# Performance work log

Hardware: AMD Instinct MI355X
Metric: run time of the kernel (lower is better)

The kernel has to match this reference:

```python
import jax, jax.numpy as jnp
import numpy as np

B, R, D, P = 32, 512, 256, 5532  # images, rois/image, feat dim, num_pids
NEG_INF = -1e30

def setup_inputs() -> dict:
    key = jax.random.key(0)
    k1, k2, k3 = jax.random.split(key, 3)
    inputs = jax.random.normal(k1, (B * R, D), dtype=jnp.float32)
    cls_scores = jax.random.uniform(k2, (B * R, 1), dtype=jnp.float32)
    roi_label = jax.random.randint(k3, (B, R), 0, P + 1)  # 0 = background -> label -1
    return {"inputs": inputs, "cls_scores": cls_scores, "roi_label": roi_label}

def reference(inputs, cls_scores, roi_label):
    x = (inputs * cls_scores).reshape(B, R, D)          # scale features by cls score
    label = roi_label - 1                               # [B,R], -1 = background
    valid = label >= 0                                  # keep labeled ROIs only
    lbl = jnp.where(valid, label, 0)

    # per-image per-pid mean prototypes via one segmented reduction
    seg = (jnp.arange(B)[:, None] * P + lbl).reshape(-1)             # [B*R]
    w = valid.reshape(-1).astype(x.dtype)
    sums = jax.ops.segment_sum(x.reshape(-1, D) * w[:, None], seg, num_segments=B * P)
    counts = jax.ops.segment_sum(w, seg, num_segments=B * P)          # [B*P]
    proto = sums / jnp.maximum(counts, 1.0)[:, None]
    proto = proto / jnp.maximum(jnp.linalg.norm(proto, axis=-1, keepdims=True), 1e-12)
    proto = jax.lax.stop_gradient(proto).reshape(B, P, D)            # .detach() in torch
    present = (counts > 0).reshape(B, P)                              # unique labels per image

    # project each ROI feature onto its image's prototypes
    logits = jnp.einsum('brd,bpd->brp', x, proto)                     # [B,R,P]
    logits = jnp.where(present[:, None, :], logits, NEG_INF)          # softmax over unique labels only
    logp = jax.nn.log_softmax(logits, axis=-1)
    nll = -jnp.take_along_axis(logp, lbl[..., None], axis=-1)[..., 0] # [B,R]
    nll = jnp.where(valid, nll, 0.0)
    n_valid = jnp.maximum(jnp.sum(valid).astype(x.dtype), 1.0)
    return jnp.sum(nll) / n_valid
```

## Files before the change

### kernel.cpp

```cpp
#include <hip/hip_runtime.h>
#include <math.h>

#define Bn 32
#define Rn 512
#define Dn 256
#define Pn 5532
#define MAXU 512

typedef short short8 __attribute__((ext_vector_type(8)));
typedef short short4v __attribute__((ext_vector_type(4)));
typedef float floatx4 __attribute__((ext_vector_type(4)));

#define XBF_OFF    0
#define XBF_WORDS  (Bn*Rn*Dn/2)
#define PBF_OFF    (XBF_OFF + XBF_WORDS)
#define PBF_WORDS  (Bn*MAXU*Dn/2)
#define LBLC_OFF   (PBF_OFF + PBF_WORDS)
#define NUNIQ_OFF  (LBLC_OFF + Bn*Rn)
#define NVALID_OFF (NUNIQ_OFF + 32)
#define SEXP_OFF   (NVALID_OFF + 32)
#define NLL_OFF    (SEXP_OFF + Bn*Rn)
#define TK2_OFF    (NLL_OFF + 1)
#define TICK_OFF   (TK2_OFF + 1)
#define ZEROW      (Bn*Rn + 2 + 128)

__device__ __forceinline__ unsigned short bf16r(float f) {
    union { float f; unsigned int u; } c; c.f = f;
    return (unsigned short)((c.u + 0x7FFFu + ((c.u >> 16) & 1u)) >> 16);
}

__device__ __forceinline__ void async16(void* lds, const void* g) {
    auto* l3 = reinterpret_cast<__attribute__((address_space(3))) unsigned int*>(
                   reinterpret_cast<size_t>(lds));
    auto* g1 = reinterpret_cast<const __attribute__((address_space(1))) unsigned int*>(
                   reinterpret_cast<size_t>(g));
    __builtin_amdgcn_global_load_lds(g1, l3, 16, 0, 0);
}

__global__ __launch_bounds__(1024) void k1_prep(
    const float* __restrict__ inputs, const float* __restrict__ cls,
    const int* __restrict__ roi_label,
    unsigned short* __restrict__ xbf, unsigned short* __restrict__ pbf,
    int* __restrict__ lblc_arr, int* __restrict__ nuniq, int* __restrict__ nvalid_arr,
    int* __restrict__ zbase)
{
    const int flat = blockIdx.x;
    const int t = threadIdx.x;

    __shared__ int cnt_lds[Pn];
    __shared__ int cmap_lds[Pn];
    __shared__ int curs_lds[MAXU], ccnt_lds[MAXU];
    __shared__ int rlist_lds[Rn];
    __shared__ int wpres[16], wcnt[16];

    if (flat >= 32) {
        if (flat >= 33 && flat <= 49) {
            int idx = (flat - 33) * 1024 + t;
            if (idx < ZEROW) zbase[idx] = 0;
        }
        int g = (flat - 32) * 1024 + t;
        int e = g * 8;
        int row = e >> 8;
        float cw = cls[row];
        float4 v0 = *(const float4*)&inputs[e];
        float4 v1 = *(const float4*)&inputs[e + 4];
        short8 o;
        o[0] = (short)bf16r(v0.x * cw); o[1] = (short)bf16r(v0.y * cw);
        o[2] = (short)bf16r(v0.z * cw); o[3] = (short)bf16r(v0.w * cw);
        o[4] = (short)bf16r(v1.x * cw); o[5] = (short)bf16r(v1.y * cw);
        o[6] = (short)bf16r(v1.z * cw); o[7] = (short)bf16r(v1.w * cw);
        *(short8*)&xbf[e] = o;
        return;
    }

    const int b = flat;
    const int lane = t & 63, wid = t >> 6;
    for (int i = t; i < Pn; i += 1024) cnt_lds[i] = 0;
    __syncthreads();
    int mylbl = -1;
    if (t < Rn) {
        mylbl = roi_label[b * Rn + t] - 1;
        if (mylbl >= 0) atomicAdd(&cnt_lds[mylbl], 1);
    }
    __syncthreads();

    int basePres = 0, baseCnt = 0;
    for (int i0 = 0; i0 < Pn; i0 += 1024) {
        int i = i0 + t;
        int cnt = (i < Pn) ? cnt_lds[i] : 0;
        bool pres = cnt > 0;
        unsigned long long mask = __ballot(pres);
        int pfx_pres = __popcll(mask & ((1ULL << lane) - 1ULL));
        int v = cnt;
        #pragma unroll
        for (int off = 1; off < 64; off <<= 1) {
            int u = __shfl_up(v, off);
            if (lane >= off) v += u;
        }
        int pfx_cnt = v - cnt;
        if (lane == 63) { wpres[wid] = __popcll(mask); wcnt[wid] = v; }
        __syncthreads();
        int woffP = 0, totP = 0, woffC = 0, totC = 0;
        #pragma unroll
        for (int w = 0; w < 16; ++w) {
            int p = wpres[w], c = wcnt[w];
            if (w < wid) { woffP += p; woffC += c; }
            totP += p; totC += c;
        }
        if (pres) {
            int c = basePres + woffP + pfx_pres;
            cmap_lds[i] = c;
            ccnt_lds[c] = cnt;
            curs_lds[c] = baseCnt + woffC + pfx_cnt;
        }
        basePres += totP; baseCnt += totC;
        __syncthreads();
    }
    if (t < Rn) {
        int lc = (mylbl >= 0) ? cmap_lds[mylbl] : -1;
        lblc_arr[b * Rn + t] = lc;
        if (lc >= 0) {
            int pos = atomicAdd(&curs_lds[lc], 1);
            rlist_lds[pos] = t;
        }
    }
    if (t == 0) { nuniq[b] = basePres; nvalid_arr[b] = baseCnt; }
    __syncthreads();

    for (int s = wid; s < basePres; s += 16) {
        int cnt = ccnt_lds[s];
        int start = curs_lds[s] - cnt;
        float4 acc = make_float4(0.f, 0.f, 0.f, 0.f);
        for (int k = 0; k < cnt; ++k) {
            int r = rlist_lds[start + k];
            float cw = cls[b * Rn + r];
            float4 v = *(const float4*)&inputs[(size_t)(b * Rn + r) * Dn + lane * 4];
            acc.x += v.x * cw; acc.y += v.y * cw; acc.z += v.z * cw; acc.w += v.w * cw;
        }
        float inv = 1.0f / (float)cnt;
        acc.x *= inv; acc.y *= inv; acc.z *= inv; acc.w *= inv;
        float ss = acc.x*acc.x + acc.y*acc.y + acc.z*acc.z + acc.w*acc.w;
        #pragma unroll
        for (int off = 32; off > 0; off >>= 1) ss += __shfl_xor(ss, off);
        float scale = 1.0f / fmaxf(sqrtf(ss), 1e-12f);
        short4v o;
        o[0] = (short)bf16r(acc.x * scale); o[1] = (short)bf16r(acc.y * scale);
        o[2] = (short)bf16r(acc.z * scale); o[3] = (short)bf16r(acc.w * scale);
        *(short4v*)&pbf[(size_t)(b * MAXU + s) * Dn + lane * 4] = o;
    }
}

#define TRr 128
#define TCc 128
#define KCk 32

__global__ __launch_bounds__(256, 3) void k3_loss(
    const unsigned short* __restrict__ xbf, const unsigned short* __restrict__ pbf,
    const int* __restrict__ lblc_arr, const int* __restrict__ nuniq,
    float* __restrict__ sexp, float* __restrict__ nll,
    int* __restrict__ tick, int* __restrict__ ticket2,
    const int* __restrict__ nvalid_arr, float* __restrict__ out)
{
    __shared__ __align__(16) unsigned short xs[2][TRr * KCk];
    __shared__ __align__(16) unsigned short ps[2][TCc * KCk];
    __shared__ int lblc[TRr];
    __shared__ float msum[4];
    __shared__ int mflag;

    const int t = threadIdx.x;
    const int lane = t & 63, w = t >> 6;
    const int q = lane >> 4, r15 = lane & 15;
    const int rt = blockIdx.x;
    const int b = blockIdx.y;
    const int pc = blockIdx.z;
    const int roiBase = rt * TRr;
    const int U = nuniq[b];
    const int nch = (U == 0) ? 1 : ((U + TCc - 1) >> 7);
    if (pc >= nch) return;

    if (t < TRr) lblc[t] = lblc_arr[b * Rn + roiBase + t];

    int xrow[2], xg[2];
    #pragma unroll
    for (int cc = 0; cc < 2; ++cc) {
        int s = (w + cc * 4) * 64 + lane;
        xrow[cc] = s >> 2; xg[cc] = (s & 3) ^ ((xrow[cc] >> 1) & 3);
    }

    #define ISSUE(kc, buf)                                                         \
        do {                                                                       \
            async16(&xs[buf][w * 512],                                             \
                    xbf + (size_t)(b * Rn + roiBase + xrow[0]) * Dn                \
                        + (kc) * KCk + xg[0] * 8);                                 \
            async16(&xs[buf][(w + 4) * 512],                                       \
                    xbf + (size_t)(b * Rn + roiBase + xrow[1]) * Dn                \
                        + (kc) * KCk + xg[1] * 8);                                 \
            async16(&ps[buf][w * 512],                                             \
                    pbf + (size_t)(b * MAXU + pc * TCc + xrow[0]) * Dn             \
                        + (kc) * KCk + xg[0] * 8);                                 \
            async16(&ps[buf][(w + 4) * 512],                                       \
                    pbf + (size_t)(b * MAXU + pc * TCc + xrow[1]) * Dn             \
                        + (kc) * KCk + xg[1] * 8);                                 \
        } while (0)

    ISSUE(0, 0);

    floatx4 acc[8][2];
    #pragma unroll
    for (int mt = 0; mt < 8; ++mt)
        #pragma unroll
        for (int nt = 0; nt < 2; ++nt) acc[mt][nt] = (floatx4)0.f;

    for (int kc = 0; kc < Dn / KCk; ++kc) {
        const int cur = kc & 1;
        __syncthreads();
        if (kc < Dn / KCk - 1) ISSUE(kc + 1, cur ^ 1);

        short8 bb[2];
        #pragma unroll
        for (int nt = 0; nt < 2; ++nt) {
            int row = w * 32 + nt * 16 + r15;
            int off = row * KCk + ((q ^ ((row >> 1) & 3)) * 8);
            bb[nt] = *(const short8*)&ps[cur][off];
        }
        #pragma unroll
        for (int mt = 0; mt < 8; ++mt) {
            int row = mt * 16 + r15;
            int off = row * KCk + ((q ^ ((row >> 1) & 3)) * 8);
            short8 a = *(const short8*)&xs[cur][off];
            acc[mt][0] = __builtin_amdgcn_mfma_f32_16x16x32_bf16(a, bb[0], acc[mt][0], 0, 0, 0);
            acc[mt][1] = __builtin_amdgcn_mfma_f32_16x16x32_bf16(a, bb[1], acc[mt][1], 0, 0, 0);
        }
    }
    #undef ISSUE

    const int c0 = pc * TCc + w * 32 + r15;
    const int c1 = c0 + 16;
    const bool v0 = c0 < U, v1 = c1 < U;
    float dsum = 0.f;
    #pragma unroll
    for (int mt = 0; mt < 8; ++mt)
        #pragma unroll
        for (int reg = 0; reg < 4; ++reg) {
            int mloc = mt * 16 + q * 4 + reg;
            float d0 = acc[mt][0][reg], d1 = acc[mt][1][reg];
            int lc = lblc[mloc];
            if (v0 && c0 == lc) dsum += d0;
            if (v1 && c1 == lc) dsum += d1;
            float es = (v0 ? __expf(d0) : 0.f) + (v1 ? __expf(d1) : 0.f);
            #pragma unroll
            for (int off = 1; off < 16; off <<= 1) es += __shfl_xor(es, off);
            if (r15 == 0) atomicAdd(&sexp[b * Rn + roiBase + mloc], es);
        }
    #pragma unroll
    for (int off = 1; off < 64; off <<= 1) dsum += __shfl_xor(dsum, off);
    if (lane == 0) msum[w] = dsum;
    __syncthreads();
    if (t == 0) {
        atomicAdd(nll, -(msum[0] + msum[1] + msum[2] + msum[3]));
        __threadfence();
        int old = atomicAdd(&tick[b * 4 + rt], 1);
        mflag = (old == nch - 1);
    }
    __syncthreads();
    if (mflag) {
        float v = 0.f;
        if (t < TRr && lblc[t] >= 0)
            v = __logf(atomicAdd(&sexp[b * Rn + roiBase + t], 0.0f));
        #pragma unroll
        for (int off = 1; off < 64; off <<= 1) v += __shfl_xor(v, off);
        if (lane == 0) msum[w] = v;
        __syncthreads();
        if (t == 0) {
            atomicAdd(nll, msum[0] + msum[1] + msum[2] + msum[3]);
            __threadfence();
            int t2 = atomicAdd(ticket2, 1);
            if (t2 == 127) {
                float total = atomicAdd(nll, 0.0f);
                int nv = 0;
                for (int bb = 0; bb < Bn; ++bb) nv += nvalid_arr[bb];
                out[0] = total / fmaxf((float)nv, 1.0f);
            }
        }
    }
}

extern "C" void kernel_launch(void* const* d_in, const int* in_sizes, int n_in,
                              void* d_out, int out_size, void* d_ws, size_t ws_size,
                              hipStream_t stream) {
    const float* inputs = (const float*)d_in[0];
    const float* cls    = (const float*)d_in[1];
    const int*   roi    = (const int*)d_in[2];
    float* out = (float*)d_out;

    float* wsf = (float*)d_ws;
    int*   wsi = (int*)d_ws;
    unsigned short* xbf = (unsigned short*)(wsi + XBF_OFF);
    unsigned short* pbf = (unsigned short*)(wsi + PBF_OFF);
    int*   lblc   = wsi + LBLC_OFF;
    int*   nuniq  = wsi + NUNIQ_OFF;
    int*   nvalid = wsi + NVALID_OFF;
    float* sexp   = wsf + SEXP_OFF;
    float* nll    = wsf + NLL_OFF;
    int*   tk2    = wsi + TK2_OFF;
    int*   tick   = wsi + TICK_OFF;

    k1_prep<<<32 + 512, 1024, 0, stream>>>(inputs, cls, roi, xbf, pbf, lblc,
                                           nuniq, nvalid, wsi + SEXP_OFF);
    dim3 g(Rn / TRr, Bn, 4);
    k3_loss<<<g, 256, 0, stream>>>(xbf, pbf, lblc, nuniq, sexp, nll, tick, tk2,
                                   nvalid, out);
}
```

Before: 123.4 us.

## Split prototype averaging out of prep kernel into parallel per-prototype kernel

Moves the per-image prototype mean and normalization out of the 32 image-blocks of k1_prep into a new k2_proto kernel that runs one wavefront per (image, unique label) slot. The counts, cursors and ROI lists are written to global workspace so the new kernel can read them. This spreads the gather-reduce across many more CUs instead of 16 waves per image block. In exchange it adds an extra kernel launch, global round-trips for the metadata, and many early-exiting empty waves.

Result: faster. 103.1 us (-16.4%).

```diff
diff --git a/kernel.cpp b/kernel.cpp
--- a/kernel.cpp
+++ b/kernel.cpp
@@ -16,7 +16,10 @@
 #define PBF_OFF    (XBF_OFF + XBF_WORDS)
 #define PBF_WORDS  (Bn*MAXU*Dn/2)
 #define LBLC_OFF   (PBF_OFF + PBF_WORDS)
-#define NUNIQ_OFF  (LBLC_OFF + Bn*Rn)
+#define CCNT_OFF   (LBLC_OFF + Bn*Rn)
+#define CURS_OFF   (CCNT_OFF + Bn*MAXU)
+#define RLIST_OFF  (CURS_OFF + Bn*MAXU)
+#define NUNIQ_OFF  (RLIST_OFF + Bn*Rn)
 #define NVALID_OFF (NUNIQ_OFF + 32)
 #define SEXP_OFF   (NVALID_OFF + 32)
 #define NLL_OFF    (SEXP_OFF + Bn*Rn)
@@ -40,8 +43,9 @@
 __global__ __launch_bounds__(1024) void k1_prep(
     const float* __restrict__ inputs, const float* __restrict__ cls,
     const int* __restrict__ roi_label,
-    unsigned short* __restrict__ xbf, unsigned short* __restrict__ pbf,
-    int* __restrict__ lblc_arr, int* __restrict__ nuniq, int* __restrict__ nvalid_arr,
+    unsigned short* __restrict__ xbf,
+    int* __restrict__ lblc_arr, int* __restrict__ ccnt, int* __restrict__ cursor,
+    int* __restrict__ rlist, int* __restrict__ nuniq, int* __restrict__ nvalid_arr,
     int* __restrict__ zbase)
 {
     const int flat = blockIdx.x;
@@ -49,8 +53,7 @@
 
     __shared__ int cnt_lds[Pn];
     __shared__ int cmap_lds[Pn];
-    __shared__ int curs_lds[MAXU], ccnt_lds[MAXU];
-    __shared__ int rlist_lds[Rn];
+    __shared__ int curs_lds[MAXU];
     __shared__ int wpres[16], wcnt[16];
 
     if (flat >= 32) {
@@ -110,7 +113,7 @@
         if (pres) {
             int c = basePres + woffP + pfx_pres;
             cmap_lds[i] = c;
-            ccnt_lds[c] = cnt;
+            ccnt[b * MAXU + c] = cnt;
             curs_lds[c] = baseCnt + woffC + pfx_cnt;
         }
         basePres += totP; baseCnt += totC;
@@ -121,33 +124,45 @@
         lblc_arr[b * Rn + t] = lc;
         if (lc >= 0) {
             int pos = atomicAdd(&curs_lds[lc], 1);
-            rlist_lds[pos] = t;
-        }
-    }
+            rlist[b * Rn + pos] = t;
+        }
+    }
+    __syncthreads();
+    if (t < MAXU && t < basePres)
+        cursor[b * MAXU + t] = curs_lds[t];
     if (t == 0) { nuniq[b] = basePres; nvalid_arr[b] = baseCnt; }
-    __syncthreads();
-
-    for (int s = wid; s < basePres; s += 16) {
-        int cnt = ccnt_lds[s];
-        int start = curs_lds[s] - cnt;
-        float4 acc = make_float4(0.f, 0.f, 0.f, 0.f);
-        for (int k = 0; k < cnt; ++k) {
-            int r = rlist_lds[start + k];
-            float cw = cls[b * Rn + r];
-            float4 v = *(const float4*)&inputs[(size_t)(b * Rn + r) * Dn + lane * 4];
-            acc.x += v.x * cw; acc.y += v.y * cw; acc.z += v.z * cw; acc.w += v.w * cw;
-        }
-        float inv = 1.0f / (float)cnt;
-        acc.x *= inv; acc.y *= inv; acc.z *= inv; acc.w *= inv;
-        float ss = acc.x*acc.x + acc.y*acc.y + acc.z*acc.z + acc.w*acc.w;
-        #pragma unroll
-        for (int off = 32; off > 0; off >>= 1) ss += __shfl_xor(ss, off);
-        float scale = 1.0f / fmaxf(sqrtf(ss), 1e-12f);
-        short4v o;
-        o[0] = (short)bf16r(acc.x * scale); o[1] = (short)bf16r(acc.y * scale);
-        o[2] = (short)bf16r(acc.z * scale); o[3] = (short)bf16r(acc.w * scale);
-        *(short4v*)&pbf[(size_t)(b * MAXU + s) * Dn + lane * 4] = o;
-    }
+}
+
+__global__ __launch_bounds__(256) void k2_proto(
+    const float* __restrict__ inputs, const float* __restrict__ cls,
+    const int* __restrict__ nuniq, const int* __restrict__ ccnt,
+    const int* __restrict__ cursor, const int* __restrict__ rlist,
+    unsigned short* __restrict__ pbf)
+{
+    const int lane = threadIdx.x & 63, wv = threadIdx.x >> 6;
+    int s = blockIdx.x * 4 + wv;
+    int b = s >> 9;
+    int c = s & (MAXU - 1);
+    if (c >= nuniq[b]) return;
+    int cnt = ccnt[s];
+    int start = cursor[s] - cnt;
+    float4 acc = make_float4(0.f, 0.f, 0.f, 0.f);
+    for (int k = 0; k < cnt; ++k) {
+        int r = rlist[b * Rn + start + k];
+        float cw = cls[b * Rn + r];
+        float4 v = *(const float4*)&inputs[(size_t)(b * Rn + r) * Dn + lane * 4];
+        acc.x += v.x * cw; acc.y += v.y * cw; acc.z += v.z * cw; acc.w += v.w * cw;
+    }
+    float inv = 1.0f / (float)cnt;
+    acc.x *= inv; acc.y *= inv; acc.z *= inv; acc.w *= inv;
+    float ss = acc.x*acc.x + acc.y*acc.y + acc.z*acc.z + acc.w*acc.w;
+    #pragma unroll
+    for (int off = 32; off > 0; off >>= 1) ss += __shfl_xor(ss, off);
+    float scale = 1.0f / fmaxf(sqrtf(ss), 1e-12f);
+    short4v o;
+    o[0] = (short)bf16r(acc.x * scale); o[1] = (short)bf16r(acc.y * scale);
+    o[2] = (short)bf16r(acc.z * scale); o[3] = (short)bf16r(acc.w * scale);
+    *(short4v*)&pbf[(size_t)s * Dn + lane * 4] = o;
 }
 
 #define TRr 128
@@ -298,6 +313,9 @@
     unsigned short* xbf = (unsigned short*)(wsi + XBF_OFF);
     unsigned short* pbf = (unsigned short*)(wsi + PBF_OFF);
     int*   lblc   = wsi + LBLC_OFF;
+    int*   ccnt   = wsi + CCNT_OFF;
+    int*   cursor = wsi + CURS_OFF;
+    int*   rlist  = wsi + RLIST_OFF;
     int*   nuniq  = wsi + NUNIQ_OFF;
     int*   nvalid = wsi + NVALID_OFF;
     float* sexp   = wsf + SEXP_OFF;
@@ -305,8 +323,11 @@
     int*   tk2    = wsi + TK2_OFF;
     int*   tick   = wsi + TICK_OFF;
 
-    k1_prep<<<32 + 512, 1024, 0, stream>>>(inputs, cls, roi, xbf, pbf, lblc,
-                                           nuniq, nvalid, wsi + SEXP_OFF);
+    k1_prep<<<32 + 512, 1024, 0, stream>>>(inputs, cls, roi, xbf, lblc, ccnt,
+                                           cursor, rlist, nuniq, nvalid,
+                                           wsi + SEXP_OFF);
+    k2_proto<<<(Bn * MAXU) / 4, 256, 0, stream>>>(inputs, cls, nuniq, ccnt, cursor,
+                                                  rlist, pbf);
     dim3 g(Rn / TRr, Bn, 4);
     k3_loss<<<g, 256, 0, stream>>>(xbf, pbf, lblc, nuniq, sexp, nll, tick, tk2,
                                    nvalid, out);
```
